# Performance work log

Hardware: AMD Instinct MI355X
Metric: run time of the kernel (lower is better)

The kernel has to match this reference:

```python
import jax, jax.numpy as jnp
import numpy as np

T = 1024
H_DIM = 2048
VOCAB = 32000
N_EXPERTS = 8
TOP_K = 2
MOE_I = 1024
SHARED_I = 1024
N_HEADS = 16
Q_LORA = 512
KV_LORA = 256
NOPE = 64
ROPE = 32
V_D = 64
EPS = 1e-6
ROUTED_SCALE = 2.5
NEG = -1e30


def rmsnorm(x, w, eps=EPS):
    return x * jax.lax.rsqrt(jnp.mean(x * x, axis=-1, keepdims=True) + eps) * w


def rope_cos_sin(positions):
    inv_freq = 1.0 / (10000.0 ** (jnp.arange(0, ROPE, 2, dtype=jnp.float32) / ROPE))
    freqs = positions.astype(jnp.float32)[:, None] * inv_freq  # [T, ROPE//2]
    return jnp.cos(freqs), jnp.sin(freqs)


def apply_rope(x, cos, sin):
    # interleaved (non-neox) rotary, as DeepSeek MLA uses
    x1, x2 = x[..., 0::2], x[..., 1::2]
    return jnp.stack([x1 * cos - x2 * sin, x1 * sin + x2 * cos], axis=-1).reshape(x.shape)


def setup_inputs() -> dict:
    key = jax.random.key(0)
    ks = jax.random.split(key, 26)
    s = 0.02

    def w(k, shape, scale=s):
        return jax.random.normal(k, shape, dtype=jnp.float32) * scale

    return {
        'input_ids': jax.random.randint(ks[0], (T,), 0, VOCAB, dtype=jnp.int32),
        'positions': jnp.arange(T, dtype=jnp.int32),
        'previous_hidden_states': jax.random.normal(ks[1], (T, H_DIM), dtype=jnp.float32),
        'embed': w(ks[2], (VOCAB, H_DIM), 1.0),
        'enorm_w': jnp.ones((H_DIM,), jnp.float32),
        'hnorm_w': jnp.ones((H_DIM,), jnp.float32),
        'eh_proj_w': w(ks[3], (2 * H_DIM, H_DIM)),
        'in_ln_w': jnp.ones((H_DIM,), jnp.float32),
        'post_ln_w': jnp.ones((H_DIM,), jnp.float32),
        'q_a_w': w(ks[4], (H_DIM, Q_LORA)),
        'q_a_ln_w': jnp.ones((Q_LORA,), jnp.float32),
        'q_b_w': w(ks[5], (Q_LORA, N_HEADS * (NOPE + ROPE))),
        'kv_a_w': w(ks[6], (H_DIM, KV_LORA + ROPE)),
        'kv_a_ln_w': jnp.ones((KV_LORA,), jnp.float32),
        'kv_b_w': w(ks[7], (KV_LORA, N_HEADS * (NOPE + V_D))),
        'o_w': w(ks[8], (N_HEADS * V_D, H_DIM)),
        'gate_w': w(ks[9], (H_DIM, N_EXPERTS)),
        'gate_bias': w(ks[10], (N_EXPERTS,), 0.01),
        'expert_gate_w': w(ks[11], (N_EXPERTS, H_DIM, MOE_I)),
        'expert_up_w': w(ks[12], (N_EXPERTS, H_DIM, MOE_I)),
        'expert_down_w': w(ks[13], (N_EXPERTS, MOE_I, H_DIM)),
        'shared_gate_w': w(ks[14], (H_DIM, SHARED_I)),
        'shared_up_w': w(ks[15], (H_DIM, SHARED_I)),
        'shared_down_w': w(ks[16], (SHARED_I, H_DIM)),
    }


def reference(input_ids, positions, previous_hidden_states, embed, enorm_w, hnorm_w,
              eh_proj_w, in_ln_w, post_ln_w, q_a_w, q_a_ln_w, q_b_w, kv_a_w, kv_a_ln_w,
              kv_b_w, o_w, gate_w, gate_bias, expert_gate_w, expert_up_w, expert_down_w,
              shared_gate_w, shared_up_w, shared_down_w):
    # --- MTP head: RMSNorm x2 + concat + linear ---
    e = embed[input_ids]                                         # [T, h]
    cat_in = jnp.concatenate([rmsnorm(e, enorm_w),
                              rmsnorm(previous_hidden_states, hnorm_w)], axis=-1)
    x0 = cat_in @ eh_proj_w                                      # [T, h]

    # --- decoder layer: MLA attention ---
    resid = x0
    h = rmsnorm(x0, in_ln_w)
    q_a = rmsnorm(h @ q_a_w, q_a_ln_w)                           # [T, q_lora]
    q = (q_a @ q_b_w).reshape(T, N_HEADS, NOPE + ROPE)
    q_nope, q_pe = q[..., :NOPE], q[..., NOPE:]
    kv_a = h @ kv_a_w                                            # [T, kv_lora+rope]
    kv_c, k_pe = kv_a[:, :KV_LORA], kv_a[:, KV_LORA:]
    kv = (rmsnorm(kv_c, kv_a_ln_w) @ kv_b_w).reshape(T, N_HEADS, NOPE + V_D)
    k_nope, v = kv[..., :NOPE], kv[..., NOPE:]
    cos, sin = rope_cos_sin(positions)                           # [T, ROPE//2]
    q_pe = apply_rope(q_pe, cos[:, None, :], sin[:, None, :])
    k_pe = apply_rope(k_pe, cos, sin)
    qf = jnp.concatenate([q_nope, q_pe], axis=-1)                # [T, H, dq]
    kf = jnp.concatenate([k_nope,
                          jnp.broadcast_to(k_pe[:, None, :], (T, N_HEADS, ROPE))], axis=-1)
    scale = (NOPE + ROPE) ** -0.5
    scores = jnp.einsum('thd,shd->hts', qf, kf) * scale          # [H, T, T]
    causal = positions[:, None] >= positions[None, :]
    scores = jnp.where(causal[None], scores, NEG)
    probs = jax.nn.softmax(scores, axis=-1)
    o = jnp.einsum('hts,shv->thv', probs, v).reshape(T, N_HEADS * V_D)
    attn_out = o @ o_w

    resid = resid + attn_out
    h2 = rmsnorm(resid, post_ln_w)

    # --- DeepSeek-V3 MoE: sigmoid gating + bias-corrected top-k ---
    logits = h2 @ gate_w                                         # [T, E]
    sig = jax.nn.sigmoid(logits)
    _, top_idx = jax.lax.top_k(sig + gate_bias, TOP_K)           # selection uses bias
    top_w = jnp.take_along_axis(sig, top_idx, axis=1)            # weights from raw scores
    top_w = top_w / (jnp.sum(top_w, axis=-1, keepdims=True) + 1e-20)
    combine = (jax.nn.one_hot(top_idx, N_EXPERTS, dtype=h2.dtype)
               * top_w[..., None]).sum(axis=1) * ROUTED_SCALE    # [T, E]
    g = jnp.einsum('th,ehi->tei', h2, expert_gate_w)
    u = jnp.einsum('th,ehi->tei', h2, expert_up_w)
    d = jnp.einsum('tei,eih->teh', jax.nn.silu(g) * u, expert_down_w)
    routed = jnp.einsum('teh,te->th', d, combine)
    shared = (jax.nn.silu(h2 @ shared_gate_w) * (h2 @ shared_up_w)) @ shared_down_w
    mlp_out = routed + shared

    # module returns mtp_hidden + mtp_residual
    return mlp_out + resid
```

## Files before the change

### kernel.cpp

```cpp
#include <hip/hip_runtime.h>
#include <hip/hip_bf16.h>
#include <math.h>

constexpr int T_ = 1024;
constexpr int HDIM = 2048;
constexpr int NH = 16;
constexpr int QKD = 96;
constexpr int VD = 64;
constexpr int MAXTILES = 32;
constexpr float EPSF = 1e-6f;

using f32x4 = __attribute__((ext_vector_type(4))) float;
using s16x8 = __attribute__((ext_vector_type(8))) short;
using s16x4 = __attribute__((ext_vector_type(4))) short;

constexpr size_t OF_CATH  = 0;
constexpr size_t OF_CATL  = 2097152;
constexpr size_t OF_GACT  = 0;
constexpr size_t OF_X0    = 4194304;
constexpr size_t OF_MACT  = 6291456;
constexpr size_t OF_HH    = 8388608;
constexpr size_t OF_HL    = 9437184;
constexpr size_t OF_QRAW  = 10485760;
constexpr size_t OF_QBUF  = 11010048;
constexpr size_t OF_KVA   = 12582912;
constexpr size_t OF_KVBUF = 12877824;
constexpr size_t OF_QAH   = 14974976;
constexpr size_t OF_QAL   = 15237120;
constexpr size_t OF_KVCNH = 15499264;
constexpr size_t OF_KVCNL = 15630336;
constexpr size_t OF_QFH   = 15761408;
constexpr size_t OF_QFL   = 16547840;
constexpr size_t OF_KFH   = 17334272;
constexpr size_t OF_KFL   = 18120704;
constexpr size_t OF_VBH   = 18907136;
constexpr size_t OF_VBL   = 19431424;
constexpr size_t OF_OBH   = 19955712;
constexpr size_t OF_OBL   = 20480000;
constexpr size_t OF_ATT   = 21004288;
constexpr size_t OF_H2BF  = 23101440;
constexpr size_t OF_ROUT  = 24674304;
constexpr size_t OF_EHTH  = 24682752;
constexpr size_t OF_EHTL  = 28877056;
constexpr size_t OF_QATH  = 33071360;
constexpr size_t OF_QATL  = 33595648;
constexpr size_t OF_QBTH  = 34119936;
constexpr size_t OF_QBTL  = 34513152;
constexpr size_t OF_KVATH = 34906368;
constexpr size_t OF_KVATL = 35234048;
constexpr size_t OF_KVBTH = 35561728;
constexpr size_t OF_KVBTL = 35823872;
constexpr size_t OF_OWTH  = 36086016;
constexpr size_t OF_OWTL  = 37134592;
constexpr size_t OF_MD    = 38183168;

__device__ __forceinline__ short f2bf(float f) {
    union { float f; unsigned u; } x; x.f = f;
    unsigned r = x.u + 0x7fffu + ((x.u >> 16) & 1u);
    return (short)(r >> 16);
}
__device__ __forceinline__ float bf2f(short h) {
    union { unsigned u; float f; } x; x.u = ((unsigned)(unsigned short)h) << 16; return x.f;
}
__device__ __forceinline__ int swz(int r, int k) {
    return (r << 6) + ((((k >> 3) ^ (r & 7)) << 3) | (k & 7));
}
__device__ __forceinline__ void gload16(const void* g, void* l) {
    __builtin_amdgcn_global_load_lds((__attribute__((address_space(1))) void*)g,
                                     (__attribute__((address_space(3))) void*)l, 16, 0, 0);
}

__device__ __forceinline__ float block_sum(float v) {
    __shared__ float sbuf[9];
    int lane = threadIdx.x & 63;
    int wid  = threadIdx.x >> 6;
#pragma unroll
    for (int off = 32; off > 0; off >>= 1) v += __shfl_down(v, off);
    __syncthreads();
    if (lane == 0) sbuf[wid] = v;
    __syncthreads();
    if (threadIdx.x == 0) {
        float s = 0.f;
        int nw = blockDim.x >> 6;
        for (int i = 0; i < nw; i++) s += sbuf[i];
        sbuf[8] = s;
    }
    __syncthreads();
    return sbuf[8];
}

__global__ void transpose_split_kernel(const float* __restrict__ W, short* __restrict__ Whi,
                                       short* __restrict__ Wlo, int K, int N, int split) {
    __shared__ float tile[64][65];
    int k0 = blockIdx.x * 64, n0 = blockIdx.y * 64;
    int tn = threadIdx.x & 63;
    int tk4 = threadIdx.x >> 6;
#pragma unroll 4
    for (int i = 0; i < 16; i++) {
        int kk = tk4 * 16 + i;
        int gn = n0 + tn;
        tile[kk][tn] = (gn < N) ? W[(size_t)(k0 + kk) * N + gn] : 0.f;
    }
    __syncthreads();
    int on = threadIdx.x >> 2;
    int oc = threadIdx.x & 3;
#pragma unroll 4
    for (int i = 0; i < 16; i++) {
        int kk = oc * 16 + i;
        float v = tile[kk][on];
        short hh = f2bf(v);
        size_t o = (size_t)(n0 + on) * K + k0 + kk;
        Whi[o] = hh;
        if (split) Wlo[o] = f2bf(v - bf2f(hh));
    }
}

__global__ void embed_cat_kernel(const int* __restrict__ ids, const float* __restrict__ embed,
                                 const float* __restrict__ enorm, const float* __restrict__ prev,
                                 const float* __restrict__ hnorm, short* __restrict__ ch,
                                 short* __restrict__ cl) {
    int t = blockIdx.x;
    const float* e = embed + (size_t)ids[t] * HDIM;
    float ss = 0.f;
    for (int i = threadIdx.x; i < HDIM; i += blockDim.x) { float v = e[i]; ss += v * v; }
    float r = rsqrtf(block_sum(ss) / HDIM + EPSF);
    for (int i = threadIdx.x; i < HDIM; i += blockDim.x) {
        float v = e[i] * r * enorm[i];
        short hh = f2bf(v);
        ch[(size_t)t * 4096 + i] = hh;
        cl[(size_t)t * 4096 + i] = f2bf(v - bf2f(hh));
    }
    const float* p = prev + (size_t)t * HDIM;
    ss = 0.f;
    for (int i = threadIdx.x; i < HDIM; i += blockDim.x) { float v = p[i]; ss += v * v; }
    r = rsqrtf(block_sum(ss) / HDIM + EPSF);
    for (int i = threadIdx.x; i < HDIM; i += blockDim.x) {
        float v = p[i] * r * hnorm[i];
        short hh = f2bf(v);
        ch[(size_t)t * 4096 + 2048 + i] = hh;
        cl[(size_t)t * 4096 + 2048 + i] = f2bf(v - bf2f(hh));
    }
}

__global__ void rmsnorm_kernel(const float* __restrict__ in, int in_stride, int width,
                               const float* __restrict__ w, float* __restrict__ outf,
                               short* __restrict__ outh, short* __restrict__ outl, int out_stride) {
    int t = blockIdx.x;
    const float* x = in + (size_t)t * in_stride;
    float ss = 0.f;
    for (int i = threadIdx.x; i < width; i += blockDim.x) { float v = x[i]; ss += v * v; }
    float r = rsqrtf(block_sum(ss) / width + EPSF);
    size_t ob = (size_t)t * out_stride;
    for (int i = threadIdx.x; i < width; i += blockDim.x) {
        float v = x[i] * r * w[i];
        if (outf) outf[ob + i] = v;
        if (outh) {
            short hh = f2bf(v);
            outh[ob + i] = hh;
            if (outl) outl[ob + i] = f2bf(v - bf2f(hh));
        }
    }
}

template<bool SPLIT>
__global__ __launch_bounds__(256) void gemm_planes(const short* __restrict__ Ahi, const short* __restrict__ Alo,
                                                   const short* __restrict__ Bhi, const short* __restrict__ Blo,
                                                   float* __restrict__ C, int M, int N, int K) {
    __shared__ short As[SPLIT ? 2 : 1][128 * 64];
    __shared__ short Bs[SPLIT ? 2 : 1][64 * 64];
    const int tid = threadIdx.x;
    const int lane = tid & 63, wid = tid >> 6;
    const int g = lane >> 4, li = lane & 15;
    const int wm = wid >> 1, wn = wid & 1;
    const int row0 = blockIdx.y * 128, col0 = blockIdx.x * 64;

    f32x4 acc[4][2];
#pragma unroll
    for (int mi = 0; mi < 4; mi++)
#pragma unroll
        for (int ni = 0; ni < 2; ni++)
#pragma unroll
            for (int r = 0; r < 4; r++) acc[mi][ni][r] = 0.f;

    for (int k0 = 0; k0 < K; k0 += 64) {
#pragma unroll
        for (int j = 0; j < 4; j++) {
            int blkI = wid * 4 + j;
            int cid = blkI * 64 + lane;
            int r = cid >> 3, c = (cid & 7) ^ (r & 7);
            gload16(&Ahi[(size_t)(row0 + r) * K + k0 + c * 8], &As[0][blkI * 512]);
            if constexpr (SPLIT)
                gload16(&Alo[(size_t)(row0 + r) * K + k0 + c * 8], &As[1][blkI * 512]);
        }
#pragma unroll
        for (int j = 0; j < 2; j++) {
            int blkI = wid * 2 + j;
            int cid = blkI * 64 + lane;
            int r = cid >> 3, c = (cid & 7) ^ (r & 7);
            gload16(&Bhi[(size_t)(col0 + r) * K + k0 + c * 8], &Bs[0][blkI * 512]);
            if constexpr (SPLIT)
                gload16(&Blo[(size_t)(col0 + r) * K + k0 + c * 8], &Bs[1][blkI * 512]);
        }
        __syncthreads();
#pragma unroll
        for (int kk = 0; kk < 64; kk += 32) {
            s16x8 ah[4], bh[2];
#pragma unroll
            for (int mi = 0; mi < 4; mi++) ah[mi] = *(const s16x8*)&As[0][swz(wm * 64 + mi * 16 + li, kk + g * 8)];
#pragma unroll
            for (int ni = 0; ni < 2; ni++) bh[ni] = *(const s16x8*)&Bs[0][swz(wn * 32 + ni * 16 + li, kk + g * 8)];
            if constexpr (SPLIT) {
                s16x8 al[4], bl[2];
#pragma unroll
                for (int mi = 0; mi < 4; mi++) al[mi] = *(const s16x8*)&As[1][swz(wm * 64 + mi * 16 + li, kk + g * 8)];
#pragma unroll
                for (int ni = 0; ni < 2; ni++) bl[ni] = *(const s16x8*)&Bs[1][swz(wn * 32 + ni * 16 + li, kk + g * 8)];
#pragma unroll
                for (int mi = 0; mi < 4; mi++)
#pragma unroll
                    for (int ni = 0; ni < 2; ni++) {
                        acc[mi][ni] = __builtin_amdgcn_mfma_f32_16x16x32_bf16(ah[mi], bh[ni], acc[mi][ni], 0, 0, 0);
                        acc[mi][ni] = __builtin_amdgcn_mfma_f32_16x16x32_bf16(al[mi], bh[ni], acc[mi][ni], 0, 0, 0);
                        acc[mi][ni] = __builtin_amdgcn_mfma_f32_16x16x32_bf16(ah[mi], bl[ni], acc[mi][ni], 0, 0, 0);
                    }
            } else {
#pragma unroll
                for (int mi = 0; mi < 4; mi++)
#pragma unroll
                    for (int ni = 0; ni < 2; ni++)
                        acc[mi][ni] = __builtin_amdgcn_mfma_f32_16x16x32_bf16(ah[mi], bh[ni], acc[mi][ni], 0, 0, 0);
            }
        }
        __syncthreads();
    }
#pragma unroll
    for (int mi = 0; mi < 4; mi++)
#pragma unroll
        for (int ni = 0; ni < 2; ni++) {
            int gc = col0 + wn * 32 + ni * 16 + li;
            if (gc < N) {
#pragma unroll
                for (int r = 0; r < 4; r++) {
                    int gr = row0 + wm * 64 + mi * 16 + g * 4 + r;
                    C[(size_t)gr * N + gc] = acc[mi][ni][r];
                }
            }
        }
}

__global__ __launch_bounds__(256) void moe_gateup(const short* __restrict__ Abase, const float* __restrict__ Wg,
                                                  const float* __restrict__ Wu, const float* __restrict__ Sg,
                                                  const float* __restrict__ Su, short* __restrict__ Cact,
                                                  const int4* __restrict__ tilemap, int K, int N) {
    int4 tm = tilemap[blockIdx.y];
    int nrows = tm.z;
    if (nrows == 0) return;
    const short* A = Abase + (size_t)tm.y * K;
    const float* Bg = (tm.x < 8) ? Wg + (size_t)tm.x * K * N : Sg;
    const float* Bu = (tm.x < 8) ? Wu + (size_t)tm.x * K * N : Su;

    __shared__ short As[128 * 64];
    alignas(16) __shared__ short Bgs[64][72];
    alignas(16) __shared__ short Bus[64][72];
    const int tid = threadIdx.x;
    const int lane = tid & 63, wid = tid >> 6;
    const int g = lane >> 4, li = lane & 15;
    const int wm = wid >> 1, wn = wid & 1;
    const int col0 = blockIdx.x * 64;

    f32x4 accg[4][2], accu[4][2];
#pragma unroll
    for (int mi = 0; mi < 4; mi++)
#pragma unroll
        for (int ni = 0; ni < 2; ni++)
#pragma unroll
            for (int r = 0; r < 4; r++) { accg[mi][ni][r] = 0.f; accu[mi][ni][r] = 0.f; }

    const int skb = (tid >> 4) << 2, snb = (tid & 15) << 2;

    for (int k0 = 0; k0 < K; k0 += 64) {
#pragma unroll
        for (int j = 0; j < 4; j++) {
            int blkI = wid * 4 + j;
            int cid = blkI * 64 + lane;
            int r = cid >> 3, c = (cid & 7) ^ (r & 7);
            gload16(&A[(size_t)r * K + k0 + c * 8], &As[blkI * 512]);
        }
        {
            float4 rg[4], ru[4];
#pragma unroll
            for (int kk = 0; kk < 4; kk++) {
                rg[kk] = *(const float4*)(Bg + (size_t)(k0 + skb + kk) * N + col0 + snb);
                ru[kk] = *(const float4*)(Bu + (size_t)(k0 + skb + kk) * N + col0 + snb);
            }
#pragma unroll
            for (int n = 0; n < 4; n++) {
                s16x4 wg4, wu4;
                wg4[0] = f2bf((&rg[0].x)[n]); wg4[1] = f2bf((&rg[1].x)[n]);
                wg4[2] = f2bf((&rg[2].x)[n]); wg4[3] = f2bf((&rg[3].x)[n]);
                wu4[0] = f2bf((&ru[0].x)[n]); wu4[1] = f2bf((&ru[1].x)[n]);
                wu4[2] = f2bf((&ru[2].x)[n]); wu4[3] = f2bf((&ru[3].x)[n]);
                *(s16x4*)&Bgs[snb + n][skb] = wg4;
                *(s16x4*)&Bus[snb + n][skb] = wu4;
            }
        }
        __syncthreads();
#pragma unroll
        for (int kk = 0; kk < 64; kk += 32) {
            s16x8 a[4], bg2[2], bu2[2];
#pragma unroll
            for (int mi = 0; mi < 4; mi++) a[mi] = *(const s16x8*)&As[swz(wm * 64 + mi * 16 + li, kk + g * 8)];
#pragma unroll
            for (int ni = 0; ni < 2; ni++) {
                bg2[ni] = *(const s16x8*)&Bgs[wn * 32 + ni * 16 + li][kk + g * 8];
                bu2[ni] = *(const s16x8*)&Bus[wn * 32 + ni * 16 + li][kk + g * 8];
            }
#pragma unroll
            for (int mi = 0; mi < 4; mi++)
#pragma unroll
                for (int ni = 0; ni < 2; ni++) {
                    accg[mi][ni] = __builtin_amdgcn_mfma_f32_16x16x32_bf16(a[mi], bg2[ni], accg[mi][ni], 0, 0, 0);
                    accu[mi][ni] = __builtin_amdgcn_mfma_f32_16x16x32_bf16(a[mi], bu2[ni], accu[mi][ni], 0, 0, 0);
                }
        }
        __syncthreads();
    }
#pragma unroll
    for (int mi = 0; mi < 4; mi++)
#pragma unroll
        for (int ni = 0; ni < 2; ni++) {
            int gc = col0 + wn * 32 + ni * 16 + li;
#pragma unroll
            for (int r = 0; r < 4; r++) {
                int gr = wm * 64 + mi * 16 + g * 4 + r;
                if (gr < nrows) {
                    float x = accg[mi][ni][r], u = accu[mi][ni][r];
                    Cact[(size_t)(tm.y + gr) * N + gc] = f2bf((x / (1.f + expf(-x))) * u);
                }
            }
        }
}

__global__ __launch_bounds__(256) void moe_down(const short* __restrict__ Abase, const float* __restrict__ Wall,
                                                const float* __restrict__ Sd, float* __restrict__ Cbase,
                                                const int4* __restrict__ tilemap, int K, int N) {
    int4 tm = tilemap[blockIdx.y];
    int nrows = tm.z;
    if (nrows == 0) return;
    const short* A = Abase + (size_t)tm.y * K;
    float* C = Cbase + (size_t)tm.y * N;
    const float* B = (tm.x < 8) ? Wall + (size_t)tm.x * K * N : Sd;

    __shared__ short As[128 * 64];
    alignas(16) __shared__ short Bs[64][72];
    const int tid = threadIdx.x;
    const int lane = tid & 63, wid = tid >> 6;
    const int g = lane >> 4, li = lane & 15;
    const int wm = wid >> 1, wn = wid & 1;
    const int col0 = blockIdx.x * 64;

    f32x4 acc[4][2];
#pragma unroll
    for (int mi = 0; mi < 4; mi++)
#pragma unroll
        for (int ni = 0; ni < 2; ni++)
#pragma unroll
            for (int r = 0; r < 4; r++) acc[mi][ni][r] = 0.f;

    const int skb = (tid >> 4) << 2, snb = (tid & 15) << 2;

    for (int k0 = 0; k0 < K; k0 += 64) {
#pragma unroll
        for (int j = 0; j < 4; j++) {
            int blkI = wid * 4 + j;
            int cid = blkI * 64 + lane;
            int r = cid >> 3, c = (cid & 7) ^ (r & 7);
            gload16(&A[(size_t)r * K + k0 + c * 8], &As[blkI * 512]);
        }
        {
            float4 r4[4];
#pragma unroll
            for (int kk = 0; kk < 4; kk++)
                r4[kk] = *(const float4*)(B + (size_t)(k0 + skb + kk) * N + col0 + snb);
#pragma unroll
            for (int n = 0; n < 4; n++) {
                s16x4 w;
                w[0] = f2bf((&r4[0].x)[n]); w[1] = f2bf((&r4[1].x)[n]);
                w[2] = f2bf((&r4[2].x)[n]); w[3] = f2bf((&r4[3].x)[n]);
                *(s16x4*)&Bs[snb + n][skb] = w;
            }
        }
        __syncthreads();
#pragma unroll
        for (int kk = 0; kk < 64; kk += 32) {
            s16x8 a[4], b[2];
#pragma unroll
            for (int mi = 0; mi < 4; mi++) a[mi] = *(const s16x8*)&As[swz(wm * 64 + mi * 16 + li, kk + g * 8)];
#pragma unroll
            for (int ni = 0; ni < 2; ni++) b[ni] = *(const s16x8*)&Bs[wn * 32 + ni * 16 + li][kk + g * 8];
#pragma unroll
            for (int mi = 0; mi < 4; mi++)
#pragma unroll
                for (int ni = 0; ni < 2; ni++)
                    acc[mi][ni] = __builtin_amdgcn_mfma_f32_16x16x32_bf16(a[mi], b[ni], acc[mi][ni], 0, 0, 0);
        }
        __syncthreads();
    }
#pragma unroll
    for (int mi = 0; mi < 4; mi++)
#pragma unroll
        for (int ni = 0; ni < 2; ni++) {
            int gc = col0 + wn * 32 + ni * 16 + li;
#pragma unroll
            for (int r = 0; r < 4; r++) {
                int gr = wm * 64 + mi * 16 + g * 4 + r;
                if (gr < nrows) C[(size_t)gr * N + gc] = acc[mi][ni][r];
            }
        }
}

__global__ void prep_qkv_kernel(const float* __restrict__ q, const float* __restrict__ kva,
                                const float* __restrict__ kv, const int* __restrict__ positions,
                                short* __restrict__ qfh, short* __restrict__ qfl,
                                short* __restrict__ kfh, short* __restrict__ kfl,
                                short* __restrict__ vbh, short* __restrict__ vbl) {
    int t = blockIdx.x;
    __shared__ float cs[16], sn[16];
    if (threadIdx.x < 16) {
        float invf = powf(10000.f, -(float)(2 * threadIdx.x) / 32.f);
        float fr = (float)positions[t] * invf;
        cs[threadIdx.x] = cosf(fr);
        sn[threadIdx.x] = sinf(fr);
    }
    __syncthreads();
    for (int i = threadIdx.x; i < NH * QKD; i += blockDim.x) {
        int h = i / QKD, d = i % QKD;
        float val;
        if (d < 64) val = q[(size_t)t * 1536 + h * QKD + d];
        else {
            int r = d - 64, pr = r >> 1;
            float x1 = q[(size_t)t * 1536 + h * QKD + 64 + 2 * pr];
            float x2 = q[(size_t)t * 1536 + h * QKD + 64 + 2 * pr + 1];
            val = (r & 1) ? (x1 * sn[pr] + x2 * cs[pr]) : (x1 * cs[pr] - x2 * sn[pr]);
        }
        short hh = f2bf(val);
        qfh[(size_t)t * 1536 + i] = hh;
        qfl[(size_t)t * 1536 + i] = f2bf(val - bf2f(hh));
    }
    for (int i = threadIdx.x; i < NH * QKD; i += blockDim.x) {
        int h = i / QKD, d = i % QKD;
        float val;
        if (d < 64) val = kv[(size_t)t * 2048 + h * 128 + d];
        else {
            int r = d - 64, pr = r >> 1;
            float x1 = kva[(size_t)t * 288 + 256 + 2 * pr];
            float x2 = kva[(size_t)t * 288 + 256 + 2 * pr + 1];
            val = (r & 1) ? (x1 * sn[pr] + x2 * cs[pr]) : (x1 * cs[pr] - x2 * sn[pr]);
        }
        short hh = f2bf(val);
        kfh[(size_t)t * 1536 + i] = hh;
        kfl[(size_t)t * 1536 + i] = f2bf(val - bf2f(hh));
    }
    for (int i = threadIdx.x; i < NH * VD; i += blockDim.x) {
        int h = i / VD, d = i % VD;
        float val = kv[(size_t)t * 2048 + h * 128 + 64 + d];
        short hh = f2bf(val);
        vbh[(size_t)t * 1024 + i] = hh;
        vbl[(size_t)t * 1024 + i] = f2bf(val - bf2f(hh));
    }
}

__global__ __launch_bounds__(256) void attn_mfma_kernel(const short* __restrict__ qfh, const short* __restrict__ qfl,
                                                        const short* __restrict__ kfh, const short* __restrict__ kfl,
                                                        const short* __restrict__ vbh, const short* __restrict__ vbl,
                                                        short* __restrict__ obh, short* __restrict__ obl) {
    __shared__ short K_hi[64][104], K_lo[64][104];
    __shared__ short Vt_hi[64][72], Vt_lo[64][72];
    __shared__ short P_hi[4][16][72], P_lo[4][16][72];
    const int qt = blockIdx.x, h = blockIdx.y;
    const int tid = threadIdx.x, lane = tid & 63, w = tid >> 6;
    const int g = lane >> 4, li = lane & 15;

    s16x8 q_hi[3], q_lo[3];
    {
        const short* qb_h = qfh + (size_t)(qt * 64 + w * 16 + li) * 1536 + h * QKD;
        const short* qb_l = qfl + (size_t)(qt * 64 + w * 16 + li) * 1536 + h * QKD;
#pragma unroll
        for (int ks = 0; ks < 3; ks++) {
            q_hi[ks] = *(const s16x8*)(qb_h + ks * 32 + g * 8);
            q_lo[ks] = *(const s16x8*)(qb_l + ks * 32 + g * 8);
        }
    }

    f32x4 acc_o[4];
#pragma unroll
    for (int nc = 0; nc < 4; nc++)
#pragma unroll
        for (int r = 0; r < 4; r++) acc_o[nc][r] = 0.f;
    float m4[4] = {-1e30f, -1e30f, -1e30f, -1e30f};
    float l4[4] = {0.f, 0.f, 0.f, 0.f};
    const float scale = 0.102062072616f;

    for (int kt = 0; kt <= qt; kt++) {
#pragma unroll
        for (int it = 0; it < 3; it++) {
            int cid = it * 256 + tid;
            int key = cid / 12, c = cid % 12;
            *(s16x8*)&K_hi[key][c * 8] = *(const s16x8*)&kfh[(size_t)(kt * 64 + key) * 1536 + h * QKD + c * 8];
            *(s16x8*)&K_lo[key][c * 8] = *(const s16x8*)&kfl[(size_t)(kt * 64 + key) * 1536 + h * QKD + c * 8];
        }
#pragma unroll
        for (int it = 0; it < 2; it++) {
            int cid = it * 256 + tid;
            int key = cid >> 3, vc = cid & 7;
            s16x8 vh = *(const s16x8*)&vbh[(size_t)(kt * 64 + key) * 1024 + h * VD + vc * 8];
            s16x8 vl = *(const s16x8*)&vbl[(size_t)(kt * 64 + key) * 1024 + h * VD + vc * 8];
#pragma unroll
            for (int j = 0; j < 8; j++) {
                Vt_hi[vc * 8 + j][key] = vh[j];
                Vt_lo[vc * 8 + j][key] = vl[j];
            }
        }
        __syncthreads();

        f32x4 acc_s[4];
#pragma unroll
        for (int kc = 0; kc < 4; kc++)
#pragma unroll
            for (int r = 0; r < 4; r++) acc_s[kc][r] = 0.f;
#pragma unroll
        for (int ks = 0; ks < 3; ks++) {
#pragma unroll
            for (int kc = 0; kc < 4; kc++) {
                s16x8 kh = *(const s16x8*)&K_hi[kc * 16 + li][ks * 32 + g * 8];
                s16x8 kl = *(const s16x8*)&K_lo[kc * 16 + li][ks * 32 + g * 8];
                acc_s[kc] = __builtin_amdgcn_mfma_f32_16x16x32_bf16(q_hi[ks], kh, acc_s[kc], 0, 0, 0);
                acc_s[kc] = __builtin_amdgcn_mfma_f32_16x16x32_bf16(q_lo[ks], kh, acc_s[kc], 0, 0, 0);
                acc_s[kc] = __builtin_amdgcn_mfma_f32_16x16x32_bf16(q_hi[ks], kl, acc_s[kc], 0, 0, 0);
            }
        }
#pragma unroll
        for (int kc = 0; kc < 4; kc++)
#pragma unroll
            for (int r = 0; r < 4; r++) acc_s[kc][r] *= scale;
        if (kt == qt) {
#pragma unroll
            for (int kc = 0; kc < 4; kc++) {
                int key = kt * 64 + kc * 16 + li;
#pragma unroll
                for (int r = 0; r < 4; r++) {
                    int qr = qt * 64 + w * 16 + g * 4 + r;
                    if (key > qr) acc_s[kc][r] = -1e30f;
                }
            }
        }
        float tm4[4];
#pragma unroll
        for (int r = 0; r < 4; r++)
            tm4[r] = fmaxf(fmaxf(acc_s[0][r], acc_s[1][r]), fmaxf(acc_s[2][r], acc_s[3][r]));
#pragma unroll
        for (int off = 1; off < 16; off <<= 1)
#pragma unroll
            for (int r = 0; r < 4; r++) tm4[r] = fmaxf(tm4[r], __shfl_xor(tm4[r], off));
        float alpha[4];
#pragma unroll
        for (int r = 0; r < 4; r++) {
            float mn = fmaxf(m4[r], tm4[r]);
            alpha[r] = __expf(m4[r] - mn);
            m4[r] = mn;
        }
        float rs[4] = {0.f, 0.f, 0.f, 0.f};
#pragma unroll
        for (int kc = 0; kc < 4; kc++)
#pragma unroll
            for (int r = 0; r < 4; r++) {
                float p = __expf(acc_s[kc][r] - m4[r]);
                rs[r] += p;
                short hh = f2bf(p);
                P_hi[w][g * 4 + r][kc * 16 + li] = hh;
                P_lo[w][g * 4 + r][kc * 16 + li] = f2bf(p - bf2f(hh));
            }
#pragma unroll
        for (int off = 1; off < 16; off <<= 1)
#pragma unroll
            for (int r = 0; r < 4; r++) rs[r] += __shfl_xor(rs[r], off);
#pragma unroll
        for (int r = 0; r < 4; r++) l4[r] = l4[r] * alpha[r] + rs[r];
#pragma unroll
        for (int nc = 0; nc < 4; nc++)
#pragma unroll
            for (int r = 0; r < 4; r++) acc_o[nc][r] *= alpha[r];
#pragma unroll
        for (int ks = 0; ks < 2; ks++) {
            s16x8 ph = *(const s16x8*)&P_hi[w][li][ks * 32 + g * 8];
            s16x8 pl = *(const s16x8*)&P_lo[w][li][ks * 32 + g * 8];
#pragma unroll
            for (int nc = 0; nc < 4; nc++) {
                s16x8 vh = *(const s16x8*)&Vt_hi[nc * 16 + li][ks * 32 + g * 8];
                s16x8 vl = *(const s16x8*)&Vt_lo[nc * 16 + li][ks * 32 + g * 8];
                acc_o[nc] = __builtin_amdgcn_mfma_f32_16x16x32_bf16(ph, vh, acc_o[nc], 0, 0, 0);
                acc_o[nc] = __builtin_amdgcn_mfma_f32_16x16x32_bf16(pl, vh, acc_o[nc], 0, 0, 0);
                acc_o[nc] = __builtin_amdgcn_mfma_f32_16x16x32_bf16(ph, vl, acc_o[nc], 0, 0, 0);
            }
        }
        __syncthreads();
    }
    float inv[4];
#pragma unroll
    for (int r = 0; r < 4; r++) inv[r] = 1.f / l4[r];
#pragma unroll
    for (int nc = 0; nc < 4; nc++)
#pragma unroll
        for (int r = 0; r < 4; r++) {
            float o = acc_o[nc][r] * inv[r];
            size_t idx = (size_t)(qt * 64 + w * 16 + g * 4 + r) * 1024 + h * VD + nc * 16 + li;
            short hh = f2bf(o);
            obh[idx] = hh;
            obl[idx] = f2bf(o - bf2f(hh));
        }
}

__global__ __launch_bounds__(256) void fused_post_attn(float* __restrict__ x0, const float* __restrict__ att,
                                                       const float* __restrict__ w, const float* __restrict__ gate_w,
                                                       const float* __restrict__ gate_bias,
                                                       short* __restrict__ h2bf, int* __restrict__ topidx,
                                                       float* __restrict__ topw) {
    int t = blockIdx.x;
    float resid[8];
    float ss = 0.f;
#pragma unroll
    for (int j = 0; j < 8; j++) {
        int i = threadIdx.x + j * 256;
        float v = x0[(size_t)t * HDIM + i] + att[(size_t)t * HDIM + i];
        resid[j] = v;
        x0[(size_t)t * HDIM + i] = v;
        ss += v * v;
    }
    float r = rsqrtf(block_sum(ss) / HDIM + EPSF);
    float acc[8] = {0.f, 0.f, 0.f, 0.f, 0.f, 0.f, 0.f, 0.f};
#pragma unroll
    for (int j = 0; j < 8; j++) {
        int i = threadIdx.x + j * 256;
        float v = resid[j] * r * w[i];
        h2bf[(size_t)t * HDIM + i] = f2bf(v);
        const float* gw = gate_w + (size_t)i * 8;
        float4 g0 = *(const float4*)gw;
        float4 g1 = *(const float4*)(gw + 4);
        acc[0] = fmaf(v, g0.x, acc[0]); acc[1] = fmaf(v, g0.y, acc[1]);
        acc[2] = fmaf(v, g0.z, acc[2]); acc[3] = fmaf(v, g0.w, acc[3]);
        acc[4] = fmaf(v, g1.x, acc[4]); acc[5] = fmaf(v, g1.y, acc[5]);
        acc[6] = fmaf(v, g1.z, acc[6]); acc[7] = fmaf(v, g1.w, acc[7]);
    }
    __shared__ float logits[8];
    for (int e = 0; e < 8; e++) {
        float s = block_sum(acc[e]);
        if (threadIdx.x == 0) logits[e] = s;
    }
    __syncthreads();
    if (threadIdx.x == 0) {
        float sig[8], sc[8];
        for (int e = 0; e < 8; e++) {
            sig[e] = 1.f / (1.f + expf(-logits[e]));
            sc[e] = sig[e] + gate_bias[e];
        }
        int i0 = 0;
        for (int e = 1; e < 8; e++) if (sc[e] > sc[i0]) i0 = e;
        int i1 = -1;
        for (int e = 0; e < 8; e++) if (e != i0 && (i1 < 0 || sc[e] > sc[i1])) i1 = e;
        float w0 = sig[i0], w1 = sig[i1], s = w0 + w1 + 1e-20f;
        topidx[t * 2 + 0] = i0; topidx[t * 2 + 1] = i1;
        topw[t * 2 + 0] = w0 / s; topw[t * 2 + 1] = w1 / s;
    }
}

__global__ void sort_kernel(const int* __restrict__ topidx, int* __restrict__ sorted_t,
                            int* __restrict__ slotpos, int4* __restrict__ tilemap) {
    __shared__ int counts[8], offs[9];
    int wid = threadIdx.x >> 6, lane = threadIdx.x & 63;
    int cnt = 0;
    for (int base = 0; base < 2 * T_; base += 64) {
        int e = topidx[base + lane];
        unsigned long long m = __ballot(e == wid);
        cnt += __popcll(m);
    }
    if (lane == 0) counts[wid] = cnt;
    __syncthreads();
    if (threadIdx.x == 0) {
        offs[0] = 0;
        for (int e = 0; e < 8; e++) offs[e + 1] = offs[e] + counts[e];
    }
    __syncthreads();
    int pos = offs[wid];
    for (int base = 0; base < 2 * T_; base += 64) {
        int sl = base + lane;
        int e = topidx[sl];
        bool match = (e == wid);
        unsigned long long m = __ballot(match);
        if (match) {
            int before = __popcll(m & ((1ull << lane) - 1ull));
            int pp = pos + before;
            sorted_t[pp] = sl >> 1;
            slotpos[sl] = pp;
        }
        pos += __popcll(m);
    }
    __syncthreads();
    if (threadIdx.x == 0) {
        int nt = 0;
        for (int e = 0; e < 8; e++) {
            int c = counts[e], o = offs[e];
            for (int r = 0; r < c; r += 128) {
                tilemap[nt] = make_int4(e, o + r, min(128, c - r), 0);
                nt++;
            }
        }
        for (int r = 0; r < 8; r++) {
            tilemap[nt] = make_int4(8, 2048 + r * 128, 128, 0);
            nt++;
        }
        for (int i = nt; i < MAXTILES; i++) tilemap[i] = make_int4(0, 0, 0, 0);
    }
}

__global__ void gather_bf16_kernel(const short* __restrict__ h2bf, const int* __restrict__ sorted_t,
                                   short* __restrict__ gout) {
    int pp = blockIdx.x;
    int t = (pp < 2048) ? sorted_t[pp] : (pp - 2048);
    const s16x8* src = (const s16x8*)(h2bf + (size_t)t * HDIM);
    s16x8* dst = (s16x8*)(gout + (size_t)pp * HDIM);
    dst[threadIdx.x] = src[threadIdx.x];
}

__global__ void final_kernel(const float* __restrict__ resid, const float* __restrict__ md,
                             const int* __restrict__ slotpos, const float* __restrict__ topw,
                             float* __restrict__ out) {
    int t = blockIdx.x;
    int p0 = slotpos[t * 2 + 0], p1 = slotpos[t * 2 + 1];
    float w0 = topw[t * 2 + 0] * 2.5f, w1 = topw[t * 2 + 1] * 2.5f;
    const float* mds = md + (size_t)(2048 + t) * HDIM;
    for (int c = threadIdx.x; c < HDIM; c += blockDim.x) {
        float v = resid[(size_t)t * HDIM + c] + mds[c]
                + w0 * md[(size_t)p0 * HDIM + c] + w1 * md[(size_t)p1 * HDIM + c];
        out[(size_t)t * HDIM + c] = v;
    }
}

extern "C" void kernel_launch(void* const* d_in, const int* in_sizes, int n_in,
                              void* d_out, int out_size, void* d_ws, size_t ws_size,
                              hipStream_t stream) {
    (void)in_sizes; (void)n_in; (void)out_size; (void)ws_size;
    const int*   input_ids = (const int*)d_in[0];
    const int*   positions = (const int*)d_in[1];
    const float* prev      = (const float*)d_in[2];
    const float* embed     = (const float*)d_in[3];
    const float* enorm_w   = (const float*)d_in[4];
    const float* hnorm_w   = (const float*)d_in[5];
    const float* eh_proj_w = (const float*)d_in[6];
    const float* in_ln_w   = (const float*)d_in[7];
    const float* post_ln_w = (const float*)d_in[8];
    const float* q_a_w     = (const float*)d_in[9];
    const float* q_a_ln_w  = (const float*)d_in[10];
    const float* q_b_w     = (const float*)d_in[11];
    const float* kv_a_w    = (const float*)d_in[12];
    const float* kv_a_ln_w = (const float*)d_in[13];
    const float* kv_b_w    = (const float*)d_in[14];
    const float* o_w       = (const float*)d_in[15];
    const float* gate_w    = (const float*)d_in[16];
    const float* gate_bias = (const float*)d_in[17];
    const float* exp_g     = (const float*)d_in[18];
    const float* exp_u     = (const float*)d_in[19];
    const float* exp_d     = (const float*)d_in[20];
    const float* sh_g      = (const float*)d_in[21];
    const float* sh_u      = (const float*)d_in[22];
    const float* sh_d      = (const float*)d_in[23];
    float* out = (float*)d_out;

    float* ws = (float*)d_ws;
    short* catH  = (short*)(ws + OF_CATH);
    short* catL  = (short*)(ws + OF_CATL);
    short* gact  = (short*)(ws + OF_GACT);
    float* x0    = ws + OF_X0;
    short* mact  = (short*)(ws + OF_MACT);
    short* hH    = (short*)(ws + OF_HH);
    short* hL    = (short*)(ws + OF_HL);
    float* qraw  = ws + OF_QRAW;
    float* qbuf  = ws + OF_QBUF;
    float* kva   = ws + OF_KVA;
    float* kvbuf = ws + OF_KVBUF;
    short* qaH   = (short*)(ws + OF_QAH);
    short* qaL   = (short*)(ws + OF_QAL);
    short* kvcnH = (short*)(ws + OF_KVCNH);
    short* kvcnL = (short*)(ws + OF_KVCNL);
    short* qfH   = (short*)(ws + OF_QFH);
    short* qfL   = (short*)(ws + OF_QFL);
    short* kfH   = (short*)(ws + OF_KFH);
    short* kfL   = (short*)(ws + OF_KFL);
    short* vbH   = (short*)(ws + OF_VBH);
    short* vbL   = (short*)(ws + OF_VBL);
    short* obH   = (short*)(ws + OF_OBH);
    short* obL   = (short*)(ws + OF_OBL);
    float* att   = ws + OF_ATT;
    short* h2bf  = (short*)(ws + OF_H2BF);
    float* md    = ws + OF_MD;
    int*   ri       = (int*)(ws + OF_ROUT);
    int*   topidx   = ri;
    int*   sorted_t = ri + 2048;
    int*   slotpos  = ri + 4096;
    int4*  tilemap  = (int4*)(ri + 6144);
    float* topw     = (float*)(ri + 6144 + 4 * MAXTILES);
    short* ehTH  = (short*)(ws + OF_EHTH);
    short* ehTL  = (short*)(ws + OF_EHTL);
    short* qaTH  = (short*)(ws + OF_QATH);
    short* qaTL  = (short*)(ws + OF_QATL);
    short* qbTH  = (short*)(ws + OF_QBTH);
    short* qbTL  = (short*)(ws + OF_QBTL);
    short* kvaTH = (short*)(ws + OF_KVATH);
    short* kvaTL = (short*)(ws + OF_KVATL);
    short* kvbTH = (short*)(ws + OF_KVBTH);
    short* kvbTL = (short*)(ws + OF_KVBTL);
    short* owTH  = (short*)(ws + OF_OWTH);
    short* owTL  = (short*)(ws + OF_OWTL);

    dim3 blk(256);

    transpose_split_kernel<<<dim3(64, 32), blk, 0, stream>>>(eh_proj_w, ehTH, ehTL, 4096, 2048, 1);
    transpose_split_kernel<<<dim3(32, 8), blk, 0, stream>>>(q_a_w, qaTH, qaTL, 2048, 512, 1);
    transpose_split_kernel<<<dim3(8, 24), blk, 0, stream>>>(q_b_w, qbTH, qbTL, 512, 1536, 1);
    transpose_split_kernel<<<dim3(32, 5), blk, 0, stream>>>(kv_a_w, kvaTH, kvaTL, 2048, 288, 1);
    transpose_split_kernel<<<dim3(4, 32), blk, 0, stream>>>(kv_b_w, kvbTH, kvbTL, 256, 2048, 1);
    transpose_split_kernel<<<dim3(16, 32), blk, 0, stream>>>(o_w, owTH, owTL, 1024, 2048, 1);

    embed_cat_kernel<<<T_, blk, 0, stream>>>(input_ids, embed, enorm_w, prev, hnorm_w, catH, catL);
    gemm_planes<true><<<dim3(32, 8), blk, 0, stream>>>(catH, catL, ehTH, ehTL, x0, T_, 2048, 4096);
    rmsnorm_kernel<<<T_, blk, 0, stream>>>(x0, 2048, 2048, in_ln_w, nullptr, hH, hL, 2048);
    gemm_planes<true><<<dim3(8, 8), blk, 0, stream>>>(hH, hL, qaTH, qaTL, qraw, T_, 512, 2048);
    rmsnorm_kernel<<<T_, blk, 0, stream>>>(qraw, 512, 512, q_a_ln_w, nullptr, qaH, qaL, 512);
    gemm_planes<true><<<dim3(24, 8), blk, 0, stream>>>(qaH, qaL, qbTH, qbTL, qbuf, T_, 1536, 512);
    gemm_planes<true><<<dim3(5, 8), blk, 0, stream>>>(hH, hL, kvaTH, kvaTL, kva, T_, 288, 2048);
    rmsnorm_kernel<<<T_, blk, 0, stream>>>(kva, 288, 256, kv_a_ln_w, nullptr, kvcnH, kvcnL, 256);
    gemm_planes<true><<<dim3(32, 8), blk, 0, stream>>>(kvcnH, kvcnL, kvbTH, kvbTL, kvbuf, T_, 2048, 256);
    prep_qkv_kernel<<<T_, blk, 0, stream>>>(qbuf, kva, kvbuf, positions, qfH, qfL, kfH, kfL, vbH, vbL);
    attn_mfma_kernel<<<dim3(T_ / 64, NH), blk, 0, stream>>>(qfH, qfL, kfH, kfL, vbH, vbL, obH, obL);
    gemm_planes<true><<<dim3(32, 8), blk, 0, stream>>>(obH, obL, owTH, owTL, att, T_, 2048, 1024);
    fused_post_attn<<<T_, blk, 0, stream>>>(x0, att, post_ln_w, gate_w, gate_bias, h2bf, topidx, topw);
    sort_kernel<<<1, 512, 0, stream>>>(topidx, sorted_t, slotpos, tilemap);
    gather_bf16_kernel<<<3 * T_, blk, 0, stream>>>(h2bf, sorted_t, gact);
    moe_gateup<<<dim3(16, MAXTILES), blk, 0, stream>>>(gact, exp_g, exp_u, sh_g, sh_u, mact, tilemap, 2048, 1024);
    moe_down<<<dim3(32, MAXTILES), blk, 0, stream>>>(mact, exp_d, sh_d, md, tilemap, 1024, 2048);
    final_kernel<<<T_, blk, 0, stream>>>(x0, md, slotpos, topw, out);
}
```

Measured before the change: 608.7 us.

## Merge q_a/kv_a GEMMs, batch weight transposes, fuse gather into MoE gate-up

The six weight transpose/split launches become one multi-job kernel. The q_a and kv_a projections are concatenated into a single 800-wide GEMM whose output feeds a combined rmsnorm kernel. The separate gather kernel for routed tokens is removed, and moe_gateup now loads rows directly from h2bf through sorted_t indices. These changes cut launch count and an intermediate gather buffer round trip, at the cost of indirect row addressing in the MoE loads.

```diff
diff --git a/kernel.cpp b/kernel.cpp
--- a/kernel.cpp
+++ b/kernel.cpp
@@ -16,14 +16,11 @@
 
 constexpr size_t OF_CATH  = 0;
 constexpr size_t OF_CATL  = 2097152;
-constexpr size_t OF_GACT  = 0;
 constexpr size_t OF_X0    = 4194304;
 constexpr size_t OF_MACT  = 6291456;
 constexpr size_t OF_HH    = 8388608;
 constexpr size_t OF_HL    = 9437184;
-constexpr size_t OF_QRAW  = 10485760;
 constexpr size_t OF_QBUF  = 11010048;
-constexpr size_t OF_KVA   = 12582912;
 constexpr size_t OF_KVBUF = 12877824;
 constexpr size_t OF_QAH   = 14974976;
 constexpr size_t OF_QAL   = 15237120;
@@ -42,17 +39,16 @@
 constexpr size_t OF_ROUT  = 24674304;
 constexpr size_t OF_EHTH  = 24682752;
 constexpr size_t OF_EHTL  = 28877056;
-constexpr size_t OF_QATH  = 33071360;
-constexpr size_t OF_QATL  = 33595648;
 constexpr size_t OF_QBTH  = 34119936;
 constexpr size_t OF_QBTL  = 34513152;
-constexpr size_t OF_KVATH = 34906368;
-constexpr size_t OF_KVATL = 35234048;
 constexpr size_t OF_KVBTH = 35561728;
 constexpr size_t OF_KVBTL = 35823872;
 constexpr size_t OF_OWTH  = 36086016;
 constexpr size_t OF_OWTL  = 37134592;
 constexpr size_t OF_MD    = 38183168;
+constexpr size_t OF_QKRAW = 44474624;
+constexpr size_t OF_BATH  = 45293824;
+constexpr size_t OF_BATL  = 46145792;
 
 __device__ __forceinline__ short f2bf(float f) {
     union { float f; unsigned u; } x; x.f = f;
@@ -89,10 +85,30 @@
     return sbuf[8];
 }
 
-__global__ void transpose_split_kernel(const float* __restrict__ W, short* __restrict__ Whi,
-                                       short* __restrict__ Wlo, int K, int N, int split) {
+struct TJobs {
+    const float* W[6];
+    short* Whi[6];
+    short* Wlo[6];
+    int K[6];
+    int N[6];
+    int nbx[6];
+    int base[7];
+};
+
+__global__ void transpose_multi_kernel(TJobs J) {
+    int bid = blockIdx.x;
+    int j = 0;
+#pragma unroll
+    for (int i = 1; i < 6; i++) if (bid >= J.base[i]) j = i;
+    int local = bid - J.base[j];
+    int K = J.K[j], N = J.N[j];
+    int bx = local % J.nbx[j], by = local / J.nbx[j];
+    const float* W = J.W[j];
+    short* Whi = J.Whi[j];
+    short* Wlo = J.Wlo[j];
+
     __shared__ float tile[64][65];
-    int k0 = blockIdx.x * 64, n0 = blockIdx.y * 64;
+    int k0 = bx * 64, n0 = by * 64;
     int tn = threadIdx.x & 63;
     int tk4 = threadIdx.x >> 6;
 #pragma unroll 4
@@ -111,7 +127,7 @@
         short hh = f2bf(v);
         size_t o = (size_t)(n0 + on) * K + k0 + kk;
         Whi[o] = hh;
-        if (split) Wlo[o] = f2bf(v - bf2f(hh));
+        Wlo[o] = f2bf(v - bf2f(hh));
     }
 }
 
@@ -162,6 +178,32 @@
     }
 }
 
+__global__ void rmsnorm_qkv_kernel(const float* __restrict__ qkraw, const float* __restrict__ wq,
+                                   const float* __restrict__ wkv, short* __restrict__ qaH,
+                                   short* __restrict__ qaL, short* __restrict__ kvcnH,
+                                   short* __restrict__ kvcnL) {
+    int t = blockIdx.x;
+    const float* row = qkraw + (size_t)t * 800;
+    float ss = 0.f;
+    for (int i = threadIdx.x; i < 512; i += blockDim.x) { float v = row[i]; ss += v * v; }
+    float r = rsqrtf(block_sum(ss) / 512.f + EPSF);
+    for (int i = threadIdx.x; i < 512; i += blockDim.x) {
+        float v = row[i] * r * wq[i];
+        short hh = f2bf(v);
+        qaH[(size_t)t * 512 + i] = hh;
+        qaL[(size_t)t * 512 + i] = f2bf(v - bf2f(hh));
+    }
+    ss = 0.f;
+    for (int i = threadIdx.x; i < 256; i += blockDim.x) { float v = row[512 + i]; ss += v * v; }
+    r = rsqrtf(block_sum(ss) / 256.f + EPSF);
+    for (int i = threadIdx.x; i < 256; i += blockDim.x) {
+        float v = row[512 + i] * r * wkv[i];
+        short hh = f2bf(v);
+        kvcnH[(size_t)t * 256 + i] = hh;
+        kvcnL[(size_t)t * 256 + i] = f2bf(v - bf2f(hh));
+    }
+}
+
 template<bool SPLIT>
 __global__ __launch_bounds__(256) void gemm_planes(const short* __restrict__ Ahi, const short* __restrict__ Alo,
                                                    const short* __restrict__ Bhi, const short* __restrict__ Blo,
@@ -248,14 +290,14 @@
         }
 }
 
-__global__ __launch_bounds__(256) void moe_gateup(const short* __restrict__ Abase, const float* __restrict__ Wg,
-                                                  const float* __restrict__ Wu, const float* __restrict__ Sg,
-                                                  const float* __restrict__ Su, short* __restrict__ Cact,
-                                                  const int4* __restrict__ tilemap, int K, int N) {
+__global__ __launch_bounds__(256) void moe_gateup(const short* __restrict__ h2bf, const int* __restrict__ sorted_t,
+                                                  const float* __restrict__ Wg, const float* __restrict__ Wu,
+                                                  const float* __restrict__ Sg, const float* __restrict__ Su,
+                                                  short* __restrict__ Cact, const int4* __restrict__ tilemap,
+                                                  int K, int N) {
     int4 tm = tilemap[blockIdx.y];
     int nrows = tm.z;
     if (nrows == 0) return;
-    const short* A = Abase + (size_t)tm.y * K;
     const float* Bg = (tm.x < 8) ? Wg + (size_t)tm.x * K * N : Sg;
     const float* Bu = (tm.x < 8) ? Wu + (size_t)tm.x * K * N : Su;
 
@@ -268,6 +310,16 @@
     const int wm = wid >> 1, wn = wid & 1;
     const int col0 = blockIdx.x * 64;
 
+    int tokens[4];
+#pragma unroll
+    for (int j = 0; j < 4; j++) {
+        int blkI = wid * 4 + j;
+        int cid = blkI * 64 + lane;
+        int r = cid >> 3;
+        int slot = tm.y + r;
+        tokens[j] = (slot < 2048) ? sorted_t[slot] : (slot - 2048);
+    }
+
     f32x4 accg[4][2], accu[4][2];
 #pragma unroll
     for (int mi = 0; mi < 4; mi++)
@@ -284,7 +336,7 @@
             int blkI = wid * 4 + j;
             int cid = blkI * 64 + lane;
             int r = cid >> 3, c = (cid & 7) ^ (r & 7);
-            gload16(&A[(size_t)r * K + k0 + c * 8], &As[blkI * 512]);
+            gload16(&h2bf[(size_t)tokens[j] * K + k0 + c * 8], &As[blkI * 512]);
         }
         {
             float4 rg[4], ru[4];
@@ -419,7 +471,7 @@
         }
 }
 
-__global__ void prep_qkv_kernel(const float* __restrict__ q, const float* __restrict__ kva,
+__global__ void prep_qkv_kernel(const float* __restrict__ q, const float* __restrict__ qkraw,
                                 const float* __restrict__ kv, const int* __restrict__ positions,
                                 short* __restrict__ qfh, short* __restrict__ qfl,
                                 short* __restrict__ kfh, short* __restrict__ kfl,
@@ -453,8 +505,8 @@
         if (d < 64) val = kv[(size_t)t * 2048 + h * 128 + d];
         else {
             int r = d - 64, pr = r >> 1;
-            float x1 = kva[(size_t)t * 288 + 256 + 2 * pr];
-            float x2 = kva[(size_t)t * 288 + 256 + 2 * pr + 1];
+            float x1 = qkraw[(size_t)t * 800 + 768 + 2 * pr];
+            float x2 = qkraw[(size_t)t * 800 + 768 + 2 * pr + 1];
             val = (r & 1) ? (x1 * sn[pr] + x2 * cs[pr]) : (x1 * cs[pr] - x2 * sn[pr]);
         }
         short hh = f2bf(val);
@@ -720,15 +772,6 @@
         }
         for (int i = nt; i < MAXTILES; i++) tilemap[i] = make_int4(0, 0, 0, 0);
     }
-}
-
-__global__ void gather_bf16_kernel(const short* __restrict__ h2bf, const int* __restrict__ sorted_t,
-                                   short* __restrict__ gout) {
-    int pp = blockIdx.x;
-    int t = (pp < 2048) ? sorted_t[pp] : (pp - 2048);
-    const s16x8* src = (const s16x8*)(h2bf + (size_t)t * HDIM);
-    s16x8* dst = (s16x8*)(gout + (size_t)pp * HDIM);
-    dst[threadIdx.x] = src[threadIdx.x];
 }
 
 __global__ void final_kernel(const float* __restrict__ resid, const float* __restrict__ md,
@@ -778,14 +821,11 @@
     float* ws = (float*)d_ws;
     short* catH  = (short*)(ws + OF_CATH);
     short* catL  = (short*)(ws + OF_CATL);
-    short* gact  = (short*)(ws + OF_GACT);
     float* x0    = ws + OF_X0;
     short* mact  = (short*)(ws + OF_MACT);
     short* hH    = (short*)(ws + OF_HH);
     short* hL    = (short*)(ws + OF_HL);
-    float* qraw  = ws + OF_QRAW;
     float* qbuf  = ws + OF_QBUF;
-    float* kva   = ws + OF_KVA;
     float* kvbuf = ws + OF_KVBUF;
     short* qaH   = (short*)(ws + OF_QAH);
     short* qaL   = (short*)(ws + OF_QAL);
@@ -802,6 +842,9 @@
     float* att   = ws + OF_ATT;
     short* h2bf  = (short*)(ws + OF_H2BF);
     float* md    = ws + OF_MD;
+    float* qkraw = ws + OF_QKRAW;
+    short* batH  = (short*)(ws + OF_BATH);
+    short* batL  = (short*)(ws + OF_BATL);
     int*   ri       = (int*)(ws + OF_ROUT);
     int*   topidx   = ri;
     int*   sorted_t = ri + 2048;
@@ -810,12 +853,8 @@
     float* topw     = (float*)(ri + 6144 + 4 * MAXTILES);
     short* ehTH  = (short*)(ws + OF_EHTH);
     short* ehTL  = (short*)(ws + OF_EHTL);
-    short* qaTH  = (short*)(ws + OF_QATH);
-    short* qaTL  = (short*)(ws + OF_QATL);
     short* qbTH  = (short*)(ws + OF_QBTH);
     short* qbTL  = (short*)(ws + OF_QBTL);
-    short* kvaTH = (short*)(ws + OF_KVATH);
-    short* kvaTL = (short*)(ws + OF_KVATL);
     short* kvbTH = (short*)(ws + OF_KVBTH);
     short* kvbTL = (short*)(ws + OF_KVBTL);
     short* owTH  = (short*)(ws + OF_OWTH);
@@ -823,29 +862,32 @@
 
     dim3 blk(256);
 
-    transpose_split_kernel<<<dim3(64, 32), blk, 0, stream>>>(eh_proj_w, ehTH, ehTL, 4096, 2048, 1);
-    transpose_split_kernel<<<dim3(32, 8), blk, 0, stream>>>(q_a_w, qaTH, qaTL, 2048, 512, 1);
-    transpose_split_kernel<<<dim3(8, 24), blk, 0, stream>>>(q_b_w, qbTH, qbTL, 512, 1536, 1);
-    transpose_split_kernel<<<dim3(32, 5), blk, 0, stream>>>(kv_a_w, kvaTH, kvaTL, 2048, 288, 1);
-    transpose_split_kernel<<<dim3(4, 32), blk, 0, stream>>>(kv_b_w, kvbTH, kvbTL, 256, 2048, 1);
-    transpose_split_kernel<<<dim3(16, 32), blk, 0, stream>>>(o_w, owTH, owTL, 1024, 2048, 1);
+    TJobs J;
+    J.W[0] = eh_proj_w; J.Whi[0] = ehTH; J.Wlo[0] = ehTL; J.K[0] = 4096; J.N[0] = 2048; J.nbx[0] = 64;
+    J.W[1] = q_a_w; J.Whi[1] = batH; J.Wlo[1] = batL; J.K[1] = 2048; J.N[1] = 512; J.nbx[1] = 32;
+    J.W[2] = kv_a_w; J.Whi[2] = batH + (size_t)512 * 2048; J.Wlo[2] = batL + (size_t)512 * 2048;
+    J.K[2] = 2048; J.N[2] = 288; J.nbx[2] = 32;
+    J.W[3] = q_b_w; J.Whi[3] = qbTH; J.Wlo[3] = qbTL; J.K[3] = 512; J.N[3] = 1536; J.nbx[3] = 8;
+    J.W[4] = kv_b_w; J.Whi[4] = kvbTH; J.Wlo[4] = kvbTL; J.K[4] = 256; J.N[4] = 2048; J.nbx[4] = 4;
+    J.W[5] = o_w; J.Whi[5] = owTH; J.Wlo[5] = owTL; J.K[5] = 1024; J.N[5] = 2048; J.nbx[5] = 16;
+    int nby[6] = {32, 8, 5, 24, 32, 32};
+    J.base[0] = 0;
+    for (int i = 0; i < 6; i++) J.base[i + 1] = J.base[i] + J.nbx[i] * nby[i];
+    transpose_multi_kernel<<<J.base[6], blk, 0, stream>>>(J);
 
     embed_cat_kernel<<<T_, blk, 0, stream>>>(input_ids, embed, enorm_w, prev, hnorm_w, catH, catL);
     gemm_planes<true><<<dim3(32, 8), blk, 0, stream>>>(catH, catL, ehTH, ehTL, x0, T_, 2048, 4096);
     rmsnorm_kernel<<<T_, blk, 0, stream>>>(x0, 2048, 2048, in_ln_w, nullptr, hH, hL, 2048);
-    gemm_planes<true><<<dim3(8, 8), blk, 0, stream>>>(hH, hL, qaTH, qaTL, qraw, T_, 512, 2048);
-    rmsnorm_kernel<<<T_, blk, 0, stream>>>(qraw, 512, 512, q_a_ln_w, nullptr, qaH, qaL, 512);
+    gemm_planes<true><<<dim3(13, 8), blk, 0, stream>>>(hH, hL, batH, batL, qkraw, T_, 800, 2048);
+    rmsnorm_qkv_kernel<<<T_, blk, 0, stream>>>(qkraw, q_a_ln_w, kv_a_ln_w, qaH, qaL, kvcnH, kvcnL);
     gemm_planes<true><<<dim3(24, 8), blk, 0, stream>>>(qaH, qaL, qbTH, qbTL, qbuf, T_, 1536, 512);
-    gemm_planes<true><<<dim3(5, 8), blk, 0, stream>>>(hH, hL, kvaTH, kvaTL, kva, T_, 288, 2048);
-    rmsnorm_kernel<<<T_, blk, 0, stream>>>(kva, 288, 256, kv_a_ln_w, nullptr, kvcnH, kvcnL, 256);
     gemm_planes<true><<<dim3(32, 8), blk, 0, stream>>>(kvcnH, kvcnL, kvbTH, kvbTL, kvbuf, T_, 2048, 256);
-    prep_qkv_kernel<<<T_, blk, 0, stream>>>(qbuf, kva, kvbuf, positions, qfH, qfL, kfH, kfL, vbH, vbL);
+    prep_qkv_kernel<<<T_, blk, 0, stream>>>(qbuf, qkraw, kvbuf, positions, qfH, qfL, kfH, kfL, vbH, vbL);
     attn_mfma_kernel<<<dim3(T_ / 64, NH), blk, 0, stream>>>(qfH, qfL, kfH, kfL, vbH, vbL, obH, obL);
     gemm_planes<true><<<dim3(32, 8), blk, 0, stream>>>(obH, obL, owTH, owTL, att, T_, 2048, 1024);
     fused_post_attn<<<T_, blk, 0, stream>>>(x0, att, post_ln_w, gate_w, gate_bias, h2bf, topidx, topw);
     sort_kernel<<<1, 512, 0, stream>>>(topidx, sorted_t, slotpos, tilemap);
-    gather_bf16_kernel<<<3 * T_, blk, 0, stream>>>(h2bf, sorted_t, gact);
-    moe_gateup<<<dim3(16, MAXTILES), blk, 0, stream>>>(gact, exp_g, exp_u, sh_g, sh_u, mact, tilemap, 2048, 1024);
+    moe_gateup<<<dim3(16, MAXTILES), blk, 0, stream>>>(h2bf, sorted_t, exp_g, exp_u, sh_g, sh_u, mact, tilemap, 2048, 1024);
     moe_down<<<dim3(32, MAXTILES), blk, 0, stream>>>(mact, exp_d, sh_d, md, tilemap, 1024, 2048);
     final_kernel<<<T_, blk, 0, stream>>>(x0, md, slotpos, topw, out);
 }
```

Result: faster. 538.7 us (-11.5%).
